# Kernel optimization log

Measured on AMD Instinct MI355X. Metric: run time of the kernel, lower is better.

The kernel has to match this reference:

```python
import jax, jax.numpy as jnp
import numpy as np

EMBED_DIM = 64
N_NODES = 1024
LEAKY_SLOPE = 0.01  # torch.nn.LeakyReLU default


def setup_inputs() -> dict:
    key = jax.random.key(0)
    ks = jax.random.split(key, 7)
    F = EMBED_DIM
    emb = jax.random.normal(ks[0], (2, N_NODES, F), dtype=jnp.float32)
    # MLP params (stored as (in, out) so y = x @ W + b)
    W1 = jax.random.normal(ks[1], (2 * F, F), dtype=jnp.float32) / np.sqrt(2 * F)
    b1 = jnp.zeros((F,), dtype=jnp.float32)
    W2 = jax.random.normal(ks[2], (F, F // 2), dtype=jnp.float32) / np.sqrt(F)
    b2 = jnp.zeros((F // 2,), dtype=jnp.float32)
    W3 = jax.random.normal(ks[3], (F // 2, 1), dtype=jnp.float32) / np.sqrt(F // 2)
    b3 = jnp.zeros((1,), dtype=jnp.float32)
    return {"embeddings": emb, "W1": W1, "b1": b1, "W2": W2, "b2": b2, "W3": W3, "b3": b3}


def reference(embeddings, W1, b1, W2, b2, W3, b3):
    B, N, F = embeddings.shape
    # Pairwise concat without explicit repeat: instead of building [B,N,N,2F]
    # then one GEMM, split W1 into the left-half and right-half contributions
    # (concat([a,b]) @ W1 == a @ W1[:F] + b @ W1[F:]), computed on [B,N,F]
    # then broadcast-added -> avoids the 2F concat materialization.
    left = embeddings @ W1[:F]    # [B, N, F_out] contribution of node i
    right = embeddings @ W1[F:]   # [B, N, F_out] contribution of node j
    h = left[:, :, None, :] + right[:, None, :, :] + b1  # [B, N, N, F]
    h = jax.nn.leaky_relu(h, LEAKY_SLOPE)
    h = jax.nn.leaky_relu(h @ W2 + b2, LEAKY_SLOPE)       # [B, N, N, F/2]
    out = (h @ W3 + b3)[..., 0]                           # [B, N, N]
    return out
```

## Files before the change

kernel.cpp:

```cpp
#include <hip/hip_runtime.h>
#include <hip/hip_bf16.h>
#include <hip/hip_fp16.h>

#define NNODES 1024
#define FDIM   64
#define KOUT   32
#define NI     32

typedef _Float16 f16x8 __attribute__((ext_vector_type(8)));
typedef _Float16 f16x4 __attribute__((ext_vector_type(4)));
typedef float    f32x4 __attribute__((ext_vector_type(4)));

__global__ __launch_bounds__(256) void fused_pair_mlp(
    const float* __restrict__ emb, const float* __restrict__ W1,
    const float* __restrict__ b1,
    const float* __restrict__ W2, const float* __restrict__ b2,
    const float* __restrict__ W3, const float* __restrict__ b3,
    float* __restrict__ out)
{
    const int tid  = threadIdx.x;
    const int wv   = tid >> 6;
    const int ln   = tid & 63;
    const int ln16 = ln & 15;
    const int grp  = ln >> 4;

    const int b  = blockIdx.z;
    const int j0 = blockIdx.x * 64;
    const int i0 = blockIdx.y * NI;

    __shared__ _Float16 semb[96][72];
    __shared__ _Float16 lleft[NI][FDIM];
    __shared__ _Float16 rtile[64][FDIM];

    {
        const float* ebase = emb + (size_t)b * NNODES * FDIM;
#pragma unroll
        for (int q = 0; q < 6; ++q) {
            const int idx  = q * 256 + tid;
            const int row  = idx >> 4;
            const int c4   = idx & 15;
            const int grow = (row < 32) ? (i0 + row) : (j0 + row - 32);
            const float4 v = *(const float4*)(ebase + (size_t)grow * FDIM + c4 * 4);
            f16x4 hv = { (_Float16)v.x, (_Float16)v.y, (_Float16)v.z, (_Float16)v.w };
            *(f16x4*)(&semb[row][c4 * 4]) = hv;
        }
    }

    const int ow = wv * 16 + ln16;
    f16x8 bW1L[2], bW1R[2];
#pragma unroll
    for (int s = 0; s < 2; ++s)
#pragma unroll
        for (int e = 0; e < 8; ++e) {
            bW1L[s][e] = (_Float16)W1[(s * 32 + grp * 8 + e) * FDIM + ow];
            bW1R[s][e] = (_Float16)W1[(64 + s * 32 + grp * 8 + e) * FDIM + ow];
        }
    const float b1v = b1[ow];

    f16x8 aW[2][2];
#pragma unroll
    for (int t = 0; t < 2; ++t)
#pragma unroll
        for (int s = 0; s < 2; ++s)
#pragma unroll
            for (int e = 0; e < 8; ++e)
                aW[t][s][e] = (_Float16)W2[(s * 32 + grp * 8 + e) * KOUT
                                           + t * 16 + ln16];

    f32x4 c0i, c1i;
    float wa[8], wb[8];
#pragma unroll
    for (int r = 0; r < 4; ++r) {
        c0i[r] = b2[grp * 4 + r];
        c1i[r] = b2[16 + grp * 4 + r];
        const float w3lo = W3[grp * 4 + r];
        const float w3hi = W3[16 + grp * 4 + r];
        wa[r]     = 0.505f * w3lo;  wb[r]     = 0.495f * w3lo;
        wa[r + 4] = 0.505f * w3hi;  wb[r + 4] = 0.495f * w3hi;
    }
    const float bias3 = b3[0];

    __syncthreads();

#pragma unroll
    for (int mt = 0; mt < 2; ++mt) {
        const _Float16* ap = &semb[mt * 16 + ln16][grp * 8];
        const f16x8 a0 = *(const f16x8*)ap;
        const f16x8 a1 = *(const f16x8*)(ap + 32);
        f32x4 acc = {0.f, 0.f, 0.f, 0.f};
        acc = __builtin_amdgcn_mfma_f32_16x16x32_f16(a0, bW1L[0], acc, 0, 0, 0);
        acc = __builtin_amdgcn_mfma_f32_16x16x32_f16(a1, bW1L[1], acc, 0, 0, 0);
#pragma unroll
        for (int r = 0; r < 4; ++r)
            lleft[mt * 16 + grp * 4 + r][ow] = (_Float16)(acc[r] + b1v);
    }
#pragma unroll
    for (int mt = 0; mt < 4; ++mt) {
        const _Float16* ap = &semb[32 + mt * 16 + ln16][grp * 8];
        const f16x8 a0 = *(const f16x8*)ap;
        const f16x8 a1 = *(const f16x8*)(ap + 32);
        f32x4 acc = {0.f, 0.f, 0.f, 0.f};
        acc = __builtin_amdgcn_mfma_f32_16x16x32_f16(a0, bW1R[0], acc, 0, 0, 0);
        acc = __builtin_amdgcn_mfma_f32_16x16x32_f16(a1, bW1R[1], acc, 0, 0, 0);
#pragma unroll
        for (int r = 0; r < 4; ++r)
            rtile[mt * 16 + grp * 4 + r][ow] = (_Float16)acc[r];
    }

    __syncthreads();

    const int jj = j0 + wv * 16 + ln16;
    const _Float16* rp = &rtile[wv * 16 + ln16][0];
    const f16x8 r0 = *(const f16x8*)(rp + grp * 8);
    const f16x8 r1 = *(const f16x8*)(rp + 32 + grp * 8);

    const _Float16 slope = (_Float16)0.01f;

#pragma unroll 2
    for (int ii = 0; ii < NI; ++ii) {
        const _Float16* lrow = &lleft[ii][0];
        const f16x8 l0 = *(const f16x8*)(lrow + grp * 8);
        const f16x8 l1 = *(const f16x8*)(lrow + 32 + grp * 8);

        f16x8 h0 = l0 + r0;
        f16x8 h1 = l1 + r1;
        h0 = __builtin_elementwise_max(h0, h0 * slope);
        h1 = __builtin_elementwise_max(h1, h1 * slope);

        f32x4 acc0 = c0i;
        f32x4 acc1 = c1i;
        acc0 = __builtin_amdgcn_mfma_f32_16x16x32_f16(aW[0][0], h0, acc0, 0, 0, 0);
        acc0 = __builtin_amdgcn_mfma_f32_16x16x32_f16(aW[0][1], h1, acc0, 0, 0, 0);
        acc1 = __builtin_amdgcn_mfma_f32_16x16x32_f16(aW[1][0], h0, acc1, 0, 0, 0);
        acc1 = __builtin_amdgcn_mfma_f32_16x16x32_f16(aW[1][1], h1, acc1, 0, 0, 0);

        float p = 0.f;
#pragma unroll
        for (int r = 0; r < 4; ++r) {
            p = fmaf(wa[r],     acc0[r],        p);
            p = fmaf(wb[r],     fabsf(acc0[r]), p);
            p = fmaf(wa[r + 4], acc1[r],        p);
            p = fmaf(wb[r + 4], fabsf(acc1[r]), p);
        }
        p += __shfl_xor(p, 16, 64);
        p += __shfl_xor(p, 32, 64);
        if (grp == 0)
            out[((size_t)b * NNODES + (i0 + ii)) * NNODES + jj] = p + bias3;
    }
}

extern "C" void kernel_launch(void* const* d_in, const int* in_sizes, int n_in,
                              void* d_out, int out_size, void* d_ws, size_t ws_size,
                              hipStream_t stream) {
    const float* emb = (const float*)d_in[0];
    const float* W1  = (const float*)d_in[1];
    const float* b1  = (const float*)d_in[2];
    const float* W2  = (const float*)d_in[3];
    const float* b2  = (const float*)d_in[4];
    const float* W3  = (const float*)d_in[5];
    const float* b3  = (const float*)d_in[6];
    float* out = (float*)d_out;
    (void)d_ws; (void)ws_size;

    fused_pair_mlp<<<dim3(NNODES / 64, NNODES / NI, 2), dim3(256), 0, stream>>>(
        emb, W1, b1, W2, b2, W3, b3, out);
}
```

Baseline: 26.07 us.

## Halve i-tile, stagger wave rows, spread output stores across lane groups

```diff
diff --git a/kernel.cpp b/kernel.cpp
--- a/kernel.cpp
+++ b/kernel.cpp
@@ -5,13 +5,13 @@
 #define NNODES 1024
 #define FDIM   64
 #define KOUT   32
-#define NI     32
+#define NI     16
 
 typedef _Float16 f16x8 __attribute__((ext_vector_type(8)));
 typedef _Float16 f16x4 __attribute__((ext_vector_type(4)));
 typedef float    f32x4 __attribute__((ext_vector_type(4)));
 
-__global__ __launch_bounds__(256) void fused_pair_mlp(
+__global__ __launch_bounds__(256, 4) void fused_pair_mlp(
     const float* __restrict__ emb, const float* __restrict__ W1,
     const float* __restrict__ b1,
     const float* __restrict__ W2, const float* __restrict__ b2,
@@ -28,18 +28,18 @@
     const int j0 = blockIdx.x * 64;
     const int i0 = blockIdx.y * NI;
 
-    __shared__ _Float16 semb[96][72];
+    __shared__ _Float16 semb[80][72];
     __shared__ _Float16 lleft[NI][FDIM];
     __shared__ _Float16 rtile[64][FDIM];
 
     {
         const float* ebase = emb + (size_t)b * NNODES * FDIM;
 #pragma unroll
-        for (int q = 0; q < 6; ++q) {
+        for (int q = 0; q < 5; ++q) {
             const int idx  = q * 256 + tid;
             const int row  = idx >> 4;
             const int c4   = idx & 15;
-            const int grow = (row < 32) ? (i0 + row) : (j0 + row - 32);
+            const int grow = (row < NI) ? (i0 + row) : (j0 + row - NI);
             const float4 v = *(const float4*)(ebase + (size_t)grow * FDIM + c4 * 4);
             f16x4 hv = { (_Float16)v.x, (_Float16)v.y, (_Float16)v.z, (_Float16)v.w };
             *(f16x4*)(&semb[row][c4 * 4]) = hv;
@@ -82,9 +82,8 @@
 
     __syncthreads();
 
-#pragma unroll
-    for (int mt = 0; mt < 2; ++mt) {
-        const _Float16* ap = &semb[mt * 16 + ln16][grp * 8];
+    {
+        const _Float16* ap = &semb[ln16][grp * 8];
         const f16x8 a0 = *(const f16x8*)ap;
         const f16x8 a1 = *(const f16x8*)(ap + 32);
         f32x4 acc = {0.f, 0.f, 0.f, 0.f};
@@ -92,11 +91,11 @@
         acc = __builtin_amdgcn_mfma_f32_16x16x32_f16(a1, bW1L[1], acc, 0, 0, 0);
 #pragma unroll
         for (int r = 0; r < 4; ++r)
-            lleft[mt * 16 + grp * 4 + r][ow] = (_Float16)(acc[r] + b1v);
+            lleft[grp * 4 + r][ow] = (_Float16)(acc[r] + b1v);
     }
 #pragma unroll
     for (int mt = 0; mt < 4; ++mt) {
-        const _Float16* ap = &semb[32 + mt * 16 + ln16][grp * 8];
+        const _Float16* ap = &semb[NI + mt * 16 + ln16][grp * 8];
         const f16x8 a0 = *(const f16x8*)ap;
         const f16x8 a1 = *(const f16x8*)(ap + 32);
         f32x4 acc = {0.f, 0.f, 0.f, 0.f};
@@ -116,37 +115,51 @@
 
     const _Float16 slope = (_Float16)0.01f;
 
-#pragma unroll 2
-    for (int ii = 0; ii < NI; ++ii) {
-        const _Float16* lrow = &lleft[ii][0];
-        const f16x8 l0 = *(const f16x8*)(lrow + grp * 8);
-        const f16x8 l1 = *(const f16x8*)(lrow + 32 + grp * 8);
+#define PAIR_ITER(T, PACC) do {                                               \
+    const int ii = ((T) + wv * 4) & (NI - 1);                                 \
+    const _Float16* lrow = &lleft[ii][0];                                     \
+    const f16x8 l0 = *(const f16x8*)(lrow + grp * 8);                         \
+    const f16x8 l1 = *(const f16x8*)(lrow + 32 + grp * 8);                    \
+    f16x8 h0 = l0 + r0;                                                       \
+    f16x8 h1 = l1 + r1;                                                       \
+    h0 = __builtin_elementwise_max(h0, h0 * slope);                           \
+    h1 = __builtin_elementwise_max(h1, h1 * slope);                           \
+    f32x4 acc0 = c0i;                                                         \
+    f32x4 acc1 = c1i;                                                         \
+    __builtin_amdgcn_s_setprio(1);                                            \
+    acc0 = __builtin_amdgcn_mfma_f32_16x16x32_f16(aW[0][0], h0, acc0, 0,0,0); \
+    acc0 = __builtin_amdgcn_mfma_f32_16x16x32_f16(aW[0][1], h1, acc0, 0,0,0); \
+    acc1 = __builtin_amdgcn_mfma_f32_16x16x32_f16(aW[1][0], h0, acc1, 0,0,0); \
+    acc1 = __builtin_amdgcn_mfma_f32_16x16x32_f16(aW[1][1], h1, acc1, 0,0,0); \
+    __builtin_amdgcn_s_setprio(0);                                            \
+    float pa = 0.f, pb = 0.f, pc = 0.f, pd = 0.f;                             \
+    _Pragma("unroll")                                                         \
+    for (int r = 0; r < 4; ++r) {                                             \
+        pa = fmaf(wa[r],     acc0[r],        pa);                             \
+        pb = fmaf(wb[r],     fabsf(acc0[r]), pb);                             \
+        pc = fmaf(wa[r + 4], acc1[r],        pc);                             \
+        pd = fmaf(wb[r + 4], fabsf(acc1[r]), pd);                             \
+    }                                                                         \
+    float p = (pa + pb) + (pc + pd);                                          \
+    p += __shfl_xor(p, 16, 64);                                               \
+    p += __shfl_xor(p, 32, 64);                                               \
+    PACC = p + bias3;                                                         \
+} while (0)
 
-        f16x8 h0 = l0 + r0;
-        f16x8 h1 = l1 + r1;
-        h0 = __builtin_elementwise_max(h0, h0 * slope);
-        h1 = __builtin_elementwise_max(h1, h1 * slope);
-
-        f32x4 acc0 = c0i;
-        f32x4 acc1 = c1i;
-        acc0 = __builtin_amdgcn_mfma_f32_16x16x32_f16(aW[0][0], h0, acc0, 0, 0, 0);
-        acc0 = __builtin_amdgcn_mfma_f32_16x16x32_f16(aW[0][1], h1, acc0, 0, 0, 0);
-        acc1 = __builtin_amdgcn_mfma_f32_16x16x32_f16(aW[1][0], h0, acc1, 0, 0, 0);
-        acc1 = __builtin_amdgcn_mfma_f32_16x16x32_f16(aW[1][1], h1, acc1, 0, 0, 0);
-
-        float p = 0.f;
-#pragma unroll
-        for (int r = 0; r < 4; ++r) {
-            p = fmaf(wa[r],     acc0[r],        p);
-            p = fmaf(wb[r],     fabsf(acc0[r]), p);
-            p = fmaf(wa[r + 4], acc1[r],        p);
-            p = fmaf(wb[r + 4], fabsf(acc1[r]), p);
-        }
-        p += __shfl_xor(p, 16, 64);
-        p += __shfl_xor(p, 32, 64);
-        if (grp == 0)
-            out[((size_t)b * NNODES + (i0 + ii)) * NNODES + jj] = p + bias3;
+    for (int m = 0; m < 4; ++m) {
+        float q0, q1, q2, q3;
+        PAIR_ITER(m * 4 + 0, q0);
+        PAIR_ITER(m * 4 + 1, q1);
+        PAIR_ITER(m * 4 + 2, q2);
+        PAIR_ITER(m * 4 + 3, q3);
+        const int iibase = (m * 4 + wv * 4) & (NI - 1);
+        float v = q0;
+        v = (grp == 1) ? q1 : v;
+        v = (grp == 2) ? q2 : v;
+        v = (grp == 3) ? q3 : v;
+        out[((size_t)b * NNODES + (i0 + iibase + grp)) * NNODES + jj] = v;
     }
+#undef PAIR_ITER
 }
 
 extern "C" void kernel_launch(void* const* d_in, const int* in_sizes, int n_in,
```

New measurement: 27.71 us. 1.06x slower.

## Switch pair MLP to 32x32 MFMA tiles and compute final layer via MFMA

Applied to the files above, without the earlier changes.

```diff
diff --git a/kernel.cpp b/kernel.cpp
--- a/kernel.cpp
+++ b/kernel.cpp
@@ -5,13 +5,14 @@
 #define NNODES 1024
 #define FDIM   64
 #define KOUT   32
-#define NI     32
 
 typedef _Float16 f16x8 __attribute__((ext_vector_type(8)));
 typedef _Float16 f16x4 __attribute__((ext_vector_type(4)));
-typedef float    f32x4 __attribute__((ext_vector_type(4)));
+typedef __fp16   fp16x2 __attribute__((ext_vector_type(2)));
+typedef float    f32x4  __attribute__((ext_vector_type(4)));
+typedef float    f32x16 __attribute__((ext_vector_type(16)));
 
-__global__ __launch_bounds__(256) void fused_pair_mlp(
+__global__ __launch_bounds__(256, 4) void fused_pair_mlp(
     const float* __restrict__ emb, const float* __restrict__ W1,
     const float* __restrict__ b1,
     const float* __restrict__ W2, const float* __restrict__ b2,
@@ -22,20 +23,22 @@
     const int wv   = tid >> 6;
     const int ln   = tid & 63;
     const int ln16 = ln & 15;
-    const int grp  = ln >> 4;
+    const int grp  = (ln >> 4) & 3;
+    const int j32  = ln & 31;
+    const int hh   = ln >> 5;
 
     const int b  = blockIdx.z;
-    const int j0 = blockIdx.x * 64;
-    const int i0 = blockIdx.y * NI;
+    const int j0 = blockIdx.x * 32;
+    const int i0 = blockIdx.y * 32;
 
-    __shared__ _Float16 semb[96][72];
-    __shared__ _Float16 lleft[NI][FDIM];
-    __shared__ _Float16 rtile[64][FDIM];
+    __shared__ _Float16 semb[64][72];
+    __shared__ _Float16 lleft[32][64];
+    __shared__ _Float16 rtile[32][72];
 
     {
         const float* ebase = emb + (size_t)b * NNODES * FDIM;
 #pragma unroll
-        for (int q = 0; q < 6; ++q) {
+        for (int q = 0; q < 4; ++q) {
             const int idx  = q * 256 + tid;
             const int row  = idx >> 4;
             const int c4   = idx & 15;
@@ -57,28 +60,29 @@
         }
     const float b1v = b1[ow];
 
-    f16x8 aW[2][2];
+    f16x8 aW2[4];
+#pragma unroll
+    for (int t = 0; t < 4; ++t)
+#pragma unroll
+        for (int e = 0; e < 8; ++e)
+            aW2[t][e] = (_Float16)W2[(t * 16 + hh * 8 + e) * KOUT + j32];
+
+    f16x8 a3[2];
 #pragma unroll
     for (int t = 0; t < 2; ++t)
 #pragma unroll
-        for (int s = 0; s < 2; ++s)
+        for (int e = 0; e < 8; ++e)
+            a3[t][e] = (_Float16)W3[(e & 3) + 8 * (e >> 2) + 16 * t + 4 * hh];
+
+    f32x16 cinit;
 #pragma unroll
-            for (int e = 0; e < 8; ++e)
-                aW[t][s][e] = (_Float16)W2[(s * 32 + grp * 8 + e) * KOUT
-                                           + t * 16 + ln16];
-
-    f32x4 c0i, c1i;
-    float wa[8], wb[8];
+    for (int r = 0; r < 16; ++r)
+        cinit[r] = b2[(r & 3) + 8 * (r >> 2) + 4 * hh];
+    f32x16 c3;
+    const float bias3 = b3[0];
 #pragma unroll
-    for (int r = 0; r < 4; ++r) {
-        c0i[r] = b2[grp * 4 + r];
-        c1i[r] = b2[16 + grp * 4 + r];
-        const float w3lo = W3[grp * 4 + r];
-        const float w3hi = W3[16 + grp * 4 + r];
-        wa[r]     = 0.505f * w3lo;  wb[r]     = 0.495f * w3lo;
-        wa[r + 4] = 0.505f * w3hi;  wb[r + 4] = 0.495f * w3hi;
-    }
-    const float bias3 = b3[0];
+    for (int r = 0; r < 16; ++r)
+        c3[r] = bias3;
 
     __syncthreads();
 
@@ -95,7 +99,7 @@
             lleft[mt * 16 + grp * 4 + r][ow] = (_Float16)(acc[r] + b1v);
     }
 #pragma unroll
-    for (int mt = 0; mt < 4; ++mt) {
+    for (int mt = 0; mt < 2; ++mt) {
         const _Float16* ap = &semb[32 + mt * 16 + ln16][grp * 8];
         const f16x8 a0 = *(const f16x8*)ap;
         const f16x8 a1 = *(const f16x8*)(ap + 32);
@@ -109,43 +113,51 @@
 
     __syncthreads();
 
-    const int jj = j0 + wv * 16 + ln16;
-    const _Float16* rp = &rtile[wv * 16 + ln16][0];
-    const f16x8 r0 = *(const f16x8*)(rp + grp * 8);
-    const f16x8 r1 = *(const f16x8*)(rp + 32 + grp * 8);
+    f16x8 rj[4];
+#pragma unroll
+    for (int t = 0; t < 4; ++t)
+        rj[t] = *(const f16x8*)(&rtile[j32][t * 16 + hh * 8]);
 
     const _Float16 slope = (_Float16)0.01f;
+    float pprev = 0.f;
 
 #pragma unroll 2
-    for (int ii = 0; ii < NI; ++ii) {
+    for (int q = 0; q < 8; ++q) {
+        const int ii = wv * 8 + q;
         const _Float16* lrow = &lleft[ii][0];
-        const f16x8 l0 = *(const f16x8*)(lrow + grp * 8);
-        const f16x8 l1 = *(const f16x8*)(lrow + 32 + grp * 8);
 
-        f16x8 h0 = l0 + r0;
-        f16x8 h1 = l1 + r1;
-        h0 = __builtin_elementwise_max(h0, h0 * slope);
-        h1 = __builtin_elementwise_max(h1, h1 * slope);
+        f32x16 acc = cinit;
+#pragma unroll
+        for (int t = 0; t < 4; ++t) {
+            const f16x8 l = *(const f16x8*)(lrow + t * 16 + hh * 8);
+            f16x8 x = l + rj[t];
+            x = __builtin_elementwise_max(x, x * slope);
+            acc = __builtin_amdgcn_mfma_f32_32x32x16_f16(aW2[t], x, acc, 0, 0, 0);
+        }
 
-        f32x4 acc0 = c0i;
-        f32x4 acc1 = c1i;
-        acc0 = __builtin_amdgcn_mfma_f32_16x16x32_f16(aW[0][0], h0, acc0, 0, 0, 0);
-        acc0 = __builtin_amdgcn_mfma_f32_16x16x32_f16(aW[0][1], h1, acc0, 0, 0, 0);
-        acc1 = __builtin_amdgcn_mfma_f32_16x16x32_f16(aW[1][0], h0, acc1, 0, 0, 0);
-        acc1 = __builtin_amdgcn_mfma_f32_16x16x32_f16(aW[1][1], h1, acc1, 0, 0, 0);
+        f16x8 pb0, pb1;
+#pragma unroll
+        for (int e = 0; e < 4; ++e) {
+            const fp16x2 t0 = __builtin_amdgcn_cvt_pkrtz(acc[2 * e], acc[2 * e + 1]);
+            pb0[2 * e] = (_Float16)t0[0]; pb0[2 * e + 1] = (_Float16)t0[1];
+            const fp16x2 t1 = __builtin_amdgcn_cvt_pkrtz(acc[8 + 2 * e], acc[9 + 2 * e]);
+            pb1[2 * e] = (_Float16)t1[0]; pb1[2 * e + 1] = (_Float16)t1[1];
+        }
+        pb0 = __builtin_elementwise_max(pb0, pb0 * slope);
+        pb1 = __builtin_elementwise_max(pb1, pb1 * slope);
 
-        float p = 0.f;
-#pragma unroll
-        for (int r = 0; r < 4; ++r) {
-            p = fmaf(wa[r],     acc0[r],        p);
-            p = fmaf(wb[r],     fabsf(acc0[r]), p);
-            p = fmaf(wa[r + 4], acc1[r],        p);
-            p = fmaf(wb[r + 4], fabsf(acc1[r]), p);
+        f32x16 d = c3;
+        d = __builtin_amdgcn_mfma_f32_32x32x16_f16(a3[0], pb0, d, 0, 0, 0);
+        d = __builtin_amdgcn_mfma_f32_32x32x16_f16(a3[1], pb1, d, 0, 0, 0);
+        const float p = d[0];
+
+        if (q & 1) {
+            const float v   = hh ? p : pprev;
+            const int   row = i0 + wv * 8 + (q - 1) + hh;
+            out[((size_t)b * NNODES + row) * NNODES + j0 + j32] = v;
+        } else {
+            pprev = p;
         }
-        p += __shfl_xor(p, 16, 64);
-        p += __shfl_xor(p, 32, 64);
-        if (grp == 0)
-            out[((size_t)b * NNODES + (i0 + ii)) * NNODES + jj] = p + bias3;
     }
 }
 
@@ -162,6 +174,6 @@
     float* out = (float*)d_out;
     (void)d_ws; (void)ws_size;
 
-    fused_pair_mlp<<<dim3(NNODES / 64, NNODES / NI, 2), dim3(256), 0, stream>>>(
+    fused_pair_mlp<<<dim3(NNODES / 32, NNODES / 32, 2), dim3(256), 0, stream>>>(
         emb, W1, b1, W2, b2, W3, b3, out);
 }
```

Result: no change. 26.48 us (+1.6%).
